# Optimization experiments

Hardware: AMD Instinct MI355X
Metric: run time of the kernel (lower is better)

Reference implementation:

```python
import jax, jax.numpy as jnp
import numpy as np

B, S, H = 2, 1024, 2048
NH, NKV, HD = 16, 4, 128           # heads, kv heads, head_dim
E, TOPK, NG, TOPKG, M = 8, 2, 4, 2, 512  # experts, top_k, n_group, topk_group, moe ffn dim
EPS = 1e-6
THETA = 10000.0
SCALE = HD ** -0.5
RSF = 1.0  # routed_scaling_factor


def rmsnorm(x, w):
    xf = x.astype(jnp.float32)
    var = jnp.mean(xf * xf, axis=-1, keepdims=True)
    return (w * (xf * jax.lax.rsqrt(var + EPS))).astype(x.dtype)


def rotate_half(x):
    x1, x2 = jnp.split(x, 2, axis=-1)
    return jnp.concatenate([-x2, x1], axis=-1)


def setup_inputs() -> dict:
    key = jax.random.key(0)
    ks = jax.random.split(key, 16)
    s = 0.02
    hidden_states = jax.random.normal(ks[0], (B, S, H), jnp.float32)
    pos = jnp.arange(S, dtype=jnp.float32)
    inv_freq = 1.0 / (THETA ** (jnp.arange(0, HD, 2, dtype=jnp.float32) / HD))
    freqs = jnp.outer(pos, inv_freq)                       # [S, HD/2]
    emb = jnp.concatenate([freqs, freqs], axis=-1)         # [S, HD]
    cos = jnp.broadcast_to(jnp.cos(emb)[None], (B, S, HD))
    sin = jnp.broadcast_to(jnp.sin(emb)[None], (B, S, HD))
    return {
        "hidden_states": hidden_states,
        "cos": cos,
        "sin": sin,
        "ln1_w": jnp.ones((H,), jnp.float32),
        "w_qkv": jax.random.normal(ks[1], ((NH + 2 * NKV) * HD, H), jnp.float32) * s,
        "q_ln_w": jnp.ones((HD,), jnp.float32),
        "k_ln_w": jnp.ones((HD,), jnp.float32),
        "w_dense": jax.random.normal(ks[2], (H, NH * HD), jnp.float32) * s,
        "ln2_w": jnp.ones((H,), jnp.float32),
        "gate_w": jax.random.normal(ks[3], (E, H), jnp.float32) * s,
        "gate_bias": jnp.zeros((E,), jnp.float32),
        "we_gate": jax.random.normal(ks[4], (E, M, H), jnp.float32) * s,
        "we_up": jax.random.normal(ks[5], (E, M, H), jnp.float32) * s,
        "we_down": jax.random.normal(ks[6], (E, H, M), jnp.float32) * s,
        "ws_gate": jax.random.normal(ks[7], (M, H), jnp.float32) * s,
        "ws_up": jax.random.normal(ks[8], (M, H), jnp.float32) * s,
        "ws_down": jax.random.normal(ks[9], (H, M), jnp.float32) * s,
    }


def reference(hidden_states, cos, sin, ln1_w, w_qkv, q_ln_w, k_ln_w, w_dense,
              ln2_w, gate_w, gate_bias, we_gate, we_up, we_down,
              ws_gate, ws_up, ws_down):
    # ---- attention block ----
    residual = hidden_states
    x = rmsnorm(hidden_states, ln1_w)
    qkv = jnp.einsum('bsh,oh->bso', x, w_qkv).reshape(B, S, NH + 2 * NKV, HD)
    q, k, v = jnp.split(qkv, [NH, NH + NKV], axis=2)
    q = q.transpose(0, 2, 1, 3)   # [B, NH,  S, HD]
    k = k.transpose(0, 2, 1, 3)   # [B, NKV, S, HD]
    v = v.transpose(0, 2, 1, 3)
    q = rmsnorm(q, q_ln_w)
    k = rmsnorm(k, k_ln_w)
    c, sn = cos[:, None], sin[:, None]  # [B,1,S,HD]
    q = q * c + rotate_half(q) * sn
    k = k * c + rotate_half(k) * sn
    n_rep = NH // NKV
    k = jnp.repeat(k, n_rep, axis=1)
    v = jnp.repeat(v, n_rep, axis=1)
    scores = jnp.einsum('bhqd,bhkd->bhqk', q, k) * SCALE
    attn = jax.nn.softmax(scores.astype(jnp.float32), axis=-1).astype(q.dtype)
    out = jnp.einsum('bhqk,bhkd->bhqd', attn, v)
    out = out.transpose(0, 2, 1, 3).reshape(B, S, NH * HD)
    attn_out = jnp.einsum('bso,ho->bsh', out, w_dense)
    hidden = residual + attn_out

    # ---- MoE block ----
    residual = hidden
    x = rmsnorm(hidden, ln2_w).reshape(B * S, H)
    T = B * S
    logits = jnp.einsum('th,eh->te', x.astype(jnp.float32), gate_w.astype(jnp.float32))
    scores = jax.nn.sigmoid(logits)
    scores_b = scores + gate_bias
    # group-limited routing: pick topk_group groups by sum of top-2 scores per group
    gsz = E // NG
    grp = scores_b.reshape(T, NG, gsz)
    top2 = jax.lax.top_k(grp, min(2, gsz))[0].sum(-1)      # [T, NG]
    _, gidx = jax.lax.top_k(top2, TOPKG)                   # [T, TOPKG]
    gmask = jnp.zeros((T, NG), scores.dtype).at[jnp.arange(T)[:, None], gidx].set(1.0)
    emask = jnp.repeat(gmask, gsz, axis=-1)                # [T, E]
    masked = jnp.where(emask > 0, scores_b, -jnp.inf)
    _, tidx = jax.lax.top_k(masked, TOPK)                  # [T, TOPK]
    tw = jnp.take_along_axis(scores, tidx, axis=-1)
    tw = tw / (tw.sum(-1, keepdims=True) + 1e-20) * RSF
    route = jnp.zeros((T, E), x.dtype).at[jnp.arange(T)[:, None], tidx].set(tw.astype(x.dtype))
    # dense all-expert compute, combined by (sparse) routing weights
    g = jnp.einsum('th,emh->tem', x, we_gate)
    u = jnp.einsum('th,emh->tem', x, we_up)
    he = jax.nn.silu(g) * u
    oe = jnp.einsum('tem,ehm->teh', he, we_down)
    moe = jnp.einsum('te,teh->th', route, oe)
    # shared expert
    sh = jnp.einsum('th,oh->to', jax.nn.silu(x @ ws_gate.T) * (x @ ws_up.T), ws_down)
    out = residual + (moe + sh).reshape(B, S, H)
    return out
```

## Files before the change

kernel.cpp:

```cpp
#include <hip/hip_runtime.h>
#include <cstdint>
#include <cstddef>

#define T_TOK 2048
#define H_DIM 2048
#define S_LEN 1024
#define HD 128
#define NH 16
#define NKV 4
#define QKV_O 3072
#define MM 512
#define EPS 1e-6f
#define ATT_SCALE 0.08838834764831845f

typedef __bf16 bf16x8 __attribute__((ext_vector_type(8)));
typedef __bf16 bf16x4 __attribute__((ext_vector_type(4)));
typedef float  f32x4  __attribute__((ext_vector_type(4)));

__device__ __forceinline__ __bf16 f2bf(float f) {
  unsigned u = __builtin_bit_cast(unsigned, f);
  u += 0x7fffu + ((u >> 16) & 1u);
  unsigned short h = (unsigned short)(u >> 16);
  return __builtin_bit_cast(__bf16, h);
}
__device__ __forceinline__ f32x4 fzero4() {
  f32x4 z; z[0] = 0.f; z[1] = 0.f; z[2] = 0.f; z[3] = 0.f; return z;
}
__device__ __forceinline__ void gld16(const __bf16* g, __bf16* l) {
  __builtin_amdgcn_global_load_lds(
      (const __attribute__((address_space(1))) unsigned int*)g,
      (__attribute__((address_space(3))) unsigned int*)l, 16, 0, 0);
}

__global__ __launch_bounds__(256) void wconv_k(
    const float* __restrict__ s0, const float* __restrict__ s1,
    const float* __restrict__ s2, const float* __restrict__ s3,
    const float* __restrict__ s4, const float* __restrict__ s5,
    const float* __restrict__ s6, const float* __restrict__ s7,
    __bf16* __restrict__ dst) {
  size_t e = ((size_t)blockIdx.x * 256 + threadIdx.x) * 16;
  const size_t E0 = 6291456, E1 = 10485760, E2 = 18874368, E3 = 27262976,
               E4 = 35651584, E5 = 36700160, E6 = 37748736;
  const float* src; size_t base;
  if      (e < E0) { src = s0; base = 0;  }
  else if (e < E1) { src = s1; base = E0; }
  else if (e < E2) { src = s2; base = E1; }
  else if (e < E3) { src = s3; base = E2; }
  else if (e < E4) { src = s4; base = E3; }
  else if (e < E5) { src = s5; base = E4; }
  else if (e < E6) { src = s6; base = E5; }
  else             { src = s7; base = E6; }
  const float4* sp = (const float4*)(src + (e - base));
  float4 f0 = sp[0], f1 = sp[1], f2 = sp[2], f3 = sp[3];
  bf16x8 o0, o1;
  o0[0] = f2bf(f0.x); o0[1] = f2bf(f0.y); o0[2] = f2bf(f0.z); o0[3] = f2bf(f0.w);
  o0[4] = f2bf(f1.x); o0[5] = f2bf(f1.y); o0[6] = f2bf(f1.z); o0[7] = f2bf(f1.w);
  o1[0] = f2bf(f2.x); o1[1] = f2bf(f2.y); o1[2] = f2bf(f2.z); o1[3] = f2bf(f2.w);
  o1[4] = f2bf(f3.x); o1[5] = f2bf(f3.y); o1[6] = f2bf(f3.z); o1[7] = f2bf(f3.w);
  *(bf16x8*)(dst + e) = o0;
  *(bf16x8*)(dst + e + 8) = o1;
}

__global__ __launch_bounds__(256) void rmsnorm_k(const float* __restrict__ X,
                                                 const float* __restrict__ W,
                                                 __bf16* __restrict__ Y) {
  int t = blockIdx.x;
  int tid = threadIdx.x, lane = tid & 63, wid = tid >> 6;
  const float4* row = (const float4*)(X + (size_t)t * H_DIM);
  float4 v0 = row[tid], v1 = row[tid + 256];
  float ss = v0.x*v0.x + v0.y*v0.y + v0.z*v0.z + v0.w*v0.w
           + v1.x*v1.x + v1.y*v1.y + v1.z*v1.z + v1.w*v1.w;
  #pragma unroll
  for (int m = 1; m <= 32; m <<= 1) ss += __shfl_xor(ss, m, 64);
  __shared__ float red[4];
  if (lane == 0) red[wid] = ss;
  __syncthreads();
  float tot = red[0] + red[1] + red[2] + red[3];
  float sc = rsqrtf(tot * (1.f / H_DIM) + EPS);
  const float4* wp = (const float4*)W;
  float4 w0 = wp[tid], w1 = wp[tid + 256];
  bf16x4 o;
  o[0] = f2bf(v0.x*w0.x*sc); o[1] = f2bf(v0.y*w0.y*sc);
  o[2] = f2bf(v0.z*w0.z*sc); o[3] = f2bf(v0.w*w0.w*sc);
  *(bf16x4*)&Y[(size_t)t*H_DIM + tid*4] = o;
  o[0] = f2bf(v1.x*w1.x*sc); o[1] = f2bf(v1.y*w1.y*sc);
  o[2] = f2bf(v1.z*w1.z*sc); o[3] = f2bf(v1.w*w1.w*sc);
  *(bf16x4*)&Y[(size_t)t*H_DIM + 1024 + tid*4] = o;
}

template<int MODE>
__global__ __launch_bounds__(256) void gemm64_nt(
    const __bf16* __restrict__ A, const __bf16* __restrict__ B,
    float* __restrict__ C, __bf16* __restrict__ OB,
    const float* __restrict__ resid, int N, int K) {
  int m0 = blockIdx.y * 64;
  int n0 = blockIdx.x * 128;
  __shared__ __bf16 sA[2][64 * 64];
  __shared__ __bf16 sB[2][128 * 64];
  int tid = threadIdx.x, lane = tid & 63, wid = tid >> 6;
  int quad = lane >> 4, l16 = lane & 15;
  int wm = wid & 1, wn = wid >> 1;

  const __bf16* gA[2]; const __bf16* gB[4];
  #pragma unroll
  for (int i = 0; i < 2; i++) {
    int p = tid + 256 * i;
    int row = p >> 3, sc = p & 7, gc = sc ^ (row & 7);
    gA[i] = A + (size_t)(m0 + row) * K + gc * 8;
  }
  #pragma unroll
  for (int i = 0; i < 4; i++) {
    int p = tid + 256 * i;
    int row = p >> 3, sc = p & 7, gc = sc ^ (row & 7);
    gB[i] = B + (size_t)(n0 + row) * K + gc * 8;
  }
  f32x4 acc[2][4];
  #pragma unroll
  for (int i = 0; i < 2; i++)
    #pragma unroll
    for (int j = 0; j < 4; j++) acc[i][j] = fzero4();

  auto stage = [&](int buf, int k0) {
    #pragma unroll
    for (int i = 0; i < 2; i++)
      gld16(gA[i] + k0, &sA[buf][(tid + 256 * i) * 8]);
    #pragma unroll
    for (int i = 0; i < 4; i++)
      gld16(gB[i] + k0, &sB[buf][(tid + 256 * i) * 8]);
  };
  stage(0, 0);
  int cur = 0;
  for (int k0 = 0; k0 < K; k0 += 64) {
    __syncthreads();
    if (k0 + 64 < K) stage(cur ^ 1, k0 + 64);
    #pragma unroll
    for (int ks = 0; ks < 64; ks += 32) {
      int cb = ks >> 3;
      bf16x8 aF[2], bF[4];
      #pragma unroll
      for (int mt = 0; mt < 2; mt++) {
        int row = wm * 32 + mt * 16 + l16;
        int pos = row * 8 + ((cb + quad) ^ (row & 7));
        aF[mt] = *(const bf16x8*)&sA[cur][pos * 8];
      }
      #pragma unroll
      for (int nt = 0; nt < 4; nt++) {
        int row = wn * 64 + nt * 16 + l16;
        int pos = row * 8 + ((cb + quad) ^ (row & 7));
        bF[nt] = *(const bf16x8*)&sB[cur][pos * 8];
      }
      #pragma unroll
      for (int mt = 0; mt < 2; mt++)
        #pragma unroll
        for (int nt = 0; nt < 4; nt++)
          acc[mt][nt] = __builtin_amdgcn_mfma_f32_16x16x32_bf16(
              aF[mt], bF[nt], acc[mt][nt], 0, 0, 0);
    }
    cur ^= 1;
  }
  #pragma unroll
  for (int mt = 0; mt < 2; mt++) {
    #pragma unroll
    for (int nt = 0; nt < 4; nt++) {
      #pragma unroll
      for (int r = 0; r < 4; r++) {
        int grow = m0 + wm*32 + mt*16 + quad*4 + r;
        int gcol = n0 + wn*64 + nt*16 + l16;
        float val = acc[mt][nt][r];
        if (MODE == 0) {
          OB[(size_t)grow * N + gcol] = f2bf(val);
        } else {
          C[(size_t)grow * H_DIM + gcol] = val + resid[(size_t)grow * H_DIM + gcol];
        }
      }
    }
  }
}

__global__ __launch_bounds__(256) void gemm_down(
    const __bf16* __restrict__ A, const __bf16* __restrict__ B,
    const __bf16* __restrict__ B2, __bf16* __restrict__ OB,
    const int* __restrict__ list, const signed char* __restrict__ jsl,
    const int* __restrict__ cnt) {
  int e  = blockIdx.z;
  int ne = (e == 8) ? T_TOK : cnt[e];
  int m0 = blockIdx.y * 128;
  if (m0 >= ne) return;
  int n0 = blockIdx.x * 128;
  const __bf16* Ab = A + (size_t)e * T_TOK * MM;
  const __bf16* Bb = (e < 8) ? B + (size_t)e * H_DIM * MM : B2;
  const int K = MM;
  __shared__ __bf16 sA[2][128 * 64];
  __shared__ __bf16 sB[2][128 * 64];
  int tid = threadIdx.x, lane = tid & 63, wid = tid >> 6;
  int quad = lane >> 4, l16 = lane & 15;
  int wm = wid & 1, wn = wid >> 1;

  const __bf16* gA[4]; const __bf16* gB[4];
  #pragma unroll
  for (int i = 0; i < 4; i++) {
    int p = tid + 256 * i;
    int row = p >> 3, sc = p & 7, gc = sc ^ (row & 7);
    gA[i] = Ab + (size_t)(m0 + row) * K + gc * 8;
    gB[i] = Bb + (size_t)(n0 + row) * K + gc * 8;
  }
  f32x4 acc[4][4];
  #pragma unroll
  for (int i = 0; i < 4; i++)
    #pragma unroll
    for (int j = 0; j < 4; j++) acc[i][j] = fzero4();

  auto stage = [&](int buf, int k0) {
    #pragma unroll
    for (int i = 0; i < 4; i++) {
      gld16(gA[i] + k0, &sA[buf][(tid + 256 * i) * 8]);
      gld16(gB[i] + k0, &sB[buf][(tid + 256 * i) * 8]);
    }
  };
  stage(0, 0);
  int cur = 0;
  for (int k0 = 0; k0 < K; k0 += 64) {
    __syncthreads();
    if (k0 + 64 < K) stage(cur ^ 1, k0 + 64);
    #pragma unroll
    for (int ks = 0; ks < 64; ks += 32) {
      int cb = ks >> 3;
      bf16x8 aF[4], bF[4];
      #pragma unroll
      for (int mt = 0; mt < 4; mt++) {
        int row = wm * 64 + mt * 16 + l16;
        int pos = row * 8 + ((cb + quad) ^ (row & 7));
        aF[mt] = *(const bf16x8*)&sA[cur][pos * 8];
      }
      #pragma unroll
      for (int nt = 0; nt < 4; nt++) {
        int row = wn * 64 + nt * 16 + l16;
        int pos = row * 8 + ((cb + quad) ^ (row & 7));
        bF[nt] = *(const bf16x8*)&sB[cur][pos * 8];
      }
      #pragma unroll
      for (int mt = 0; mt < 4; mt++)
        #pragma unroll
        for (int nt = 0; nt < 4; nt++)
          acc[mt][nt] = __builtin_amdgcn_mfma_f32_16x16x32_bf16(
              aF[mt], bF[nt], acc[mt][nt], 0, 0, 0);
    }
    cur ^= 1;
  }
  #pragma unroll
  for (int mt = 0; mt < 4; mt++) {
    #pragma unroll
    for (int nt = 0; nt < 4; nt++) {
      #pragma unroll
      for (int r = 0; r < 4; r++) {
        int grow = m0 + wm*64 + mt*16 + quad*4 + r;
        int gcol = n0 + wn*64 + nt*16 + l16;
        if (grow < ne) {
          int tk = list[e * T_TOK + grow];
          int j  = (e == 8) ? 2 : (int)jsl[e * T_TOK + grow];
          OB[((size_t)tk * 3 + j) * H_DIM + gcol] = f2bf(acc[mt][nt][r]);
        }
      }
    }
  }
}

__global__ __launch_bounds__(256) void combine_k(const __bf16* __restrict__ buf,
                                                 float* __restrict__ out) {
  int t = blockIdx.x, tid = threadIdx.x;
  const __bf16* base = buf + (size_t)t * 3 * H_DIM;
  bf16x8 v0 = *(const bf16x8*)(base + tid * 8);
  bf16x8 v1 = *(const bf16x8*)(base + H_DIM + tid * 8);
  bf16x8 v2 = *(const bf16x8*)(base + 2 * H_DIM + tid * 8);
  float* o = out + (size_t)t * H_DIM + tid * 8;
  float4 a = *(float4*)o, b = *(float4*)(o + 4);
  a.x += (float)v0[0] + (float)v1[0] + (float)v2[0];
  a.y += (float)v0[1] + (float)v1[1] + (float)v2[1];
  a.z += (float)v0[2] + (float)v1[2] + (float)v2[2];
  a.w += (float)v0[3] + (float)v1[3] + (float)v2[3];
  b.x += (float)v0[4] + (float)v1[4] + (float)v2[4];
  b.y += (float)v0[5] + (float)v1[5] + (float)v2[5];
  b.z += (float)v0[6] + (float)v1[6] + (float)v2[6];
  b.w += (float)v0[7] + (float)v1[7] + (float)v2[7];
  *(float4*)o = a; *(float4*)(o + 4) = b;
}

__global__ __launch_bounds__(256) void rope_k(
    const __bf16* __restrict__ qkv, const float* __restrict__ qlw,
    const float* __restrict__ klw, const float* __restrict__ cosp,
    const float* __restrict__ sinp, __bf16* __restrict__ qb,
    __bf16* __restrict__ kb, __bf16* __restrict__ vb) {
  int bid = blockIdx.x;
  int t = bid / 6;
  int head = (bid % 6) * 4 + (threadIdx.x >> 6);
  int b = t >> 10, s = t & 1023;
  int d = threadIdx.x & 63;
  const __bf16* src = qkv + (size_t)t * QKV_O + head * HD;
  float x1 = (float)src[d], x2 = (float)src[d + 64];
  if (head < 20) {
    float ssq = x1*x1 + x2*x2;
    #pragma unroll
    for (int m = 1; m <= 32; m <<= 1) ssq += __shfl_xor(ssq, m, 64);
    float sc = rsqrtf(ssq * (1.f / HD) + EPS);
    const float* w = (head < 16) ? qlw : klw;
    x1 = x1 * sc * w[d];
    x2 = x2 * sc * w[d + 64];
    size_t cb = (size_t)t * HD;
    float c1 = cosp[cb + d], s1 = sinp[cb + d];
    float c2 = cosp[cb + d + 64], s2 = sinp[cb + d + 64];
    float o1 = x1 * c1 - x2 * s1;
    float o2 = x2 * c2 + x1 * s2;
    if (head < 16) {
      __bf16* dst = qb + (((size_t)(b * NH + head)) * S_LEN + s) * HD;
      dst[d] = f2bf(o1); dst[d + 64] = f2bf(o2);
    } else {
      int kv = head - 16;
      __bf16* dst = kb + (((size_t)(b * NKV + kv)) * S_LEN + s) * HD;
      dst[d] = f2bf(o1); dst[d + 64] = f2bf(o2);
    }
  } else {
    int kv = head - 20;
    __bf16* dst = vb + (((size_t)(b * NKV + kv)) * S_LEN + s) * HD;
    dst[d] = src[d]; dst[d + 64] = src[d + 64];
  }
}

__global__ __launch_bounds__(256) void vtrans_k(const __bf16* __restrict__ vb,
                                                __bf16* __restrict__ vt) {
  int s0 = blockIdx.x * 64, d0 = blockIdx.y * 64, g = blockIdx.z;
  __shared__ __bf16 sT[64 * 80];
  int tid = threadIdx.x;
  const __bf16* src = vb + (size_t)g * S_LEN * HD;
  #pragma unroll
  for (int i = 0; i < 2; i++) {
    int p = tid + 256 * i;
    int rs = p >> 3, cc = p & 7;
    bf16x8 v = *(const bf16x8*)(src + (size_t)(s0 + rs) * HD + d0 + cc * 8);
    #pragma unroll
    for (int j = 0; j < 8; j++) sT[(cc * 8 + j) * 80 + rs] = v[j];
  }
  __syncthreads();
  __bf16* dst = vt + (size_t)g * HD * S_LEN;
  #pragma unroll
  for (int i = 0; i < 2; i++) {
    int p = tid + 256 * i;
    int rd = p >> 3, cs = p & 7;
    bf16x8 v = *(const bf16x8*)&sT[rd * 80 + cs * 8];
    *(bf16x8*)(dst + (size_t)(d0 + rd) * S_LEN + s0 + cs * 8) = v;
  }
}

__global__ __launch_bounds__(256) void flash_k(
    const __bf16* __restrict__ qb, const __bf16* __restrict__ kb,
    const __bf16* __restrict__ vt, __bf16* __restrict__ outb) {
  int qt = blockIdx.x, bh = blockIdx.y;
  int b = bh >> 4, h = bh & 15, kv = h >> 2;
  int tid = threadIdx.x, lane = tid & 63, wid = tid >> 6;
  int quad = lane >> 4, l16 = lane & 15;
  __shared__ __bf16 sQ[64 * 128];
  __shared__ __bf16 sKP[64 * 128];
  __shared__ __bf16 sVt[128 * 64];
  __bf16* sK = sKP;
  __bf16* sP = sKP;

  const __bf16* qsrc = qb + (((size_t)(b * NH + h)) * S_LEN + qt * 64) * HD;
  #pragma unroll
  for (int i = 0; i < 4; i++) {
    int p = tid + 256 * i;
    int row = p >> 4, sc = p & 15, gc = sc ^ (row & 7);
    gld16(qsrc + (size_t)row * HD + gc * 8, &sQ[p * 8]);
  }
  const __bf16* kbase  = kb + ((size_t)(b * NKV + kv)) * S_LEN * HD;
  const __bf16* vtbase = vt + ((size_t)(b * NKV + kv)) * HD * S_LEN;
  const __bf16* gK[4]; const __bf16* gV[4];
  #pragma unroll
  for (int i = 0; i < 4; i++) {
    int p = tid + 256 * i;
    int rowk = p >> 4, sck = p & 15, gck = sck ^ (rowk & 7);
    gK[i] = kbase + (size_t)rowk * HD + gck * 8;
    int rowv = p >> 3, scv = p & 7, gcv = scv ^ (rowv & 7);
    gV[i] = vtbase + (size_t)rowv * S_LEN + gcv * 8;
  }
  float mrow[4], lrow[4];
  #pragma unroll
  for (int r = 0; r < 4; r++) { mrow[r] = -__builtin_inff(); lrow[r] = 0.f; }
  f32x4 accO[8];
  #pragma unroll
  for (int i = 0; i < 8; i++) accO[i] = fzero4();

  for (int kt = 0; kt < 16; kt++) {
    __syncthreads();
    #pragma unroll
    for (int i = 0; i < 4; i++) {
      gld16(gK[i] + (size_t)kt * 64 * HD, &sK[(tid + 256 * i) * 8]);
      gld16(gV[i] + kt * 64, &sVt[(tid + 256 * i) * 8]);
    }
    __syncthreads();
    f32x4 accS[4];
    #pragma unroll
    for (int jt = 0; jt < 4; jt++) accS[jt] = fzero4();
    int rowA = wid * 16 + l16;
    #pragma unroll
    for (int ks2 = 0; ks2 < 4; ks2++) {
      int posA = rowA * 16 + ((ks2 * 4 + quad) ^ (rowA & 7));
      bf16x8 aF = *(const bf16x8*)&sQ[posA * 8];
      #pragma unroll
      for (int jt = 0; jt < 4; jt++) {
        int rowB = jt * 16 + l16;
        int posB = rowB * 16 + ((ks2 * 4 + quad) ^ (rowB & 7));
        bf16x8 bF = *(const bf16x8*)&sK[posB * 8];
        accS[jt] = __builtin_amdgcn_mfma_f32_16x16x32_bf16(aF, bF, accS[jt], 0, 0, 0);
      }
    }
    float alpha[4];
    #pragma unroll
    for (int r = 0; r < 4; r++) {
      float mx = -__builtin_inff();
      #pragma unroll
      for (int jt = 0; jt < 4; jt++) {
        accS[jt][r] *= ATT_SCALE;
        mx = fmaxf(mx, accS[jt][r]);
      }
      #pragma unroll
      for (int m = 1; m <= 8; m <<= 1) mx = fmaxf(mx, __shfl_xor(mx, m, 64));
      float mn = fmaxf(mrow[r], mx);
      float al = __expf(mrow[r] - mn);
      float rs = 0.f;
      #pragma unroll
      for (int jt = 0; jt < 4; jt++) {
        float p = __expf(accS[jt][r] - mn);
        accS[jt][r] = p;
        rs += p;
      }
      #pragma unroll
      for (int m = 1; m <= 8; m <<= 1) rs += __shfl_xor(rs, m, 64);
      lrow[r] = lrow[r] * al + rs;
      mrow[r] = mn;
      alpha[r] = al;
    }
    #pragma unroll
    for (int nt = 0; nt < 8; nt++)
      #pragma unroll
      for (int r = 0; r < 4; r++) accO[nt][r] *= alpha[r];
    __syncthreads();
    #pragma unroll
    for (int jt = 0; jt < 4; jt++)
      #pragma unroll
      for (int r = 0; r < 4; r++)
        sP[(wid * 16 + quad * 4 + r) * 72 + jt * 16 + l16] = f2bf(accS[jt][r]);
    __syncthreads();
    #pragma unroll
    for (int ks2 = 0; ks2 < 2; ks2++) {
      bf16x8 aF = *(const bf16x8*)&sP[(wid * 16 + l16) * 72 + ks2 * 32 + quad * 8];
      #pragma unroll
      for (int nt = 0; nt < 8; nt++) {
        int rowB = nt * 16 + l16;
        int posB = rowB * 8 + ((ks2 * 4 + quad) ^ (rowB & 7));
        bf16x8 bF = *(const bf16x8*)&sVt[posB * 8];
        accO[nt] = __builtin_amdgcn_mfma_f32_16x16x32_bf16(aF, bF, accO[nt], 0, 0, 0);
      }
    }
  }
  #pragma unroll
  for (int nt = 0; nt < 8; nt++) {
    #pragma unroll
    for (int r = 0; r < 4; r++) {
      int srow = qt * 64 + wid * 16 + quad * 4 + r;
      float val = accO[nt][r] / lrow[r];
      outb[((size_t)(b * S_LEN + srow)) * H_DIM + h * HD + nt * 16 + l16] = f2bf(val);
    }
  }
}

__global__ __launch_bounds__(256) void router_k(
    const float* __restrict__ hid, const float* __restrict__ ln2w,
    const float* __restrict__ gw, const float* __restrict__ gb,
    int* __restrict__ cnt, int* __restrict__ list, float* __restrict__ wsl,
    signed char* __restrict__ jsl) {
  int t = blockIdx.x;
  int tid = threadIdx.x, lane = tid & 63, wid = tid >> 6;
  const float4* row = (const float4*)(hid + (size_t)t * H_DIM);
  float4 v0 = row[tid], v1 = row[tid + 256];
  float ss = v0.x*v0.x + v0.y*v0.y + v0.z*v0.z + v0.w*v0.w
           + v1.x*v1.x + v1.y*v1.y + v1.z*v1.z + v1.w*v1.w;
  #pragma unroll
  for (int m = 1; m <= 32; m <<= 1) ss += __shfl_xor(ss, m, 64);
  __shared__ float red[4];
  __shared__ float lred[4][8];
  if (lane == 0) red[wid] = ss;
  __syncthreads();
  float tot = red[0] + red[1] + red[2] + red[3];
  float sc = rsqrtf(tot * (1.f / H_DIM) + EPS);
  const float4* wp = (const float4*)ln2w;
  float4 w0 = wp[tid], w1 = wp[tid + 256];
  float x0 = v0.x*w0.x*sc, x1 = v0.y*w0.y*sc, x2 = v0.z*w0.z*sc, x3 = v0.w*w0.w*sc;
  float x4 = v1.x*w1.x*sc, x5 = v1.y*w1.y*sc, x6 = v1.z*w1.z*sc, x7 = v1.w*w1.w*sc;
  float pe[8];
  #pragma unroll
  for (int e = 0; e < 8; e++) {
    const float4* gp = (const float4*)(gw + (size_t)e * H_DIM);
    float4 g0 = gp[tid], g1 = gp[tid + 256];
    float d = x0*g0.x + x1*g0.y + x2*g0.z + x3*g0.w
            + x4*g1.x + x5*g1.y + x6*g1.z + x7*g1.w;
    #pragma unroll
    for (int m = 1; m <= 32; m <<= 1) d += __shfl_xor(d, m, 64);
    pe[e] = d;
  }
  if (lane == 0) {
    #pragma unroll
    for (int e = 0; e < 8; e++) lred[wid][e] = pe[e];
  }
  __syncthreads();
  if (tid == 0) {
    float s[8], sb[8];
    #pragma unroll
    for (int e = 0; e < 8; e++) {
      float lg = lred[0][e] + lred[1][e] + lred[2][e] + lred[3][e];
      s[e] = 1.f / (1.f + __expf(-lg));
      sb[e] = s[e] + gb[e];
    }
    float gs[4];
    #pragma unroll
    for (int g = 0; g < 4; g++) gs[g] = sb[2 * g] + sb[2 * g + 1];
    int g1 = 0;
    for (int g = 1; g < 4; g++) if (gs[g] > gs[g1]) g1 = g;
    int g2 = -1;
    for (int g = 0; g < 4; g++) if (g != g1 && (g2 < 0 || gs[g] > gs[g2])) g2 = g;
    unsigned emask = (3u << (2 * g1)) | (3u << (2 * g2));
    int e1 = -1;
    for (int e = 0; e < 8; e++) if (((emask >> e) & 1u) && (e1 < 0 || sb[e] > sb[e1])) e1 = e;
    int e2 = -1;
    for (int e = 0; e < 8; e++) if (((emask >> e) & 1u) && e != e1 && (e2 < 0 || sb[e] > sb[e2])) e2 = e;
    float w1s = s[e1], w2s = s[e2];
    float dn = w1s + w2s + 1e-20f;
    w1s /= dn; w2s /= dn;
    int p1 = atomicAdd(&cnt[e1], 1);
    list[e1 * T_TOK + p1] = t; wsl[e1 * T_TOK + p1] = w1s; jsl[e1 * T_TOK + p1] = 0;
    int p2 = atomicAdd(&cnt[e2], 1);
    list[e2 * T_TOK + p2] = t; wsl[e2 * T_TOK + p2] = w2s; jsl[e2 * T_TOK + p2] = 1;
    list[8 * T_TOK + t] = t; wsl[8 * T_TOK + t] = 1.f;
  }
}

__global__ __launch_bounds__(256) void gemm_gateup(
    const __bf16* __restrict__ X, const __bf16* __restrict__ weg,
    const __bf16* __restrict__ weu, const __bf16* __restrict__ wsg,
    const __bf16* __restrict__ wsu, const int* __restrict__ list,
    const float* __restrict__ wsl, const int* __restrict__ cnt,
    __bf16* __restrict__ he) {
  int e = blockIdx.z;
  int ne = (e == 8) ? T_TOK : cnt[e];
  int m0 = blockIdx.y * 128;
  if (m0 >= ne) return;
  int n0 = blockIdx.x * 64;
  const __bf16* bg = (e < 8) ? weg + (size_t)e * MM * H_DIM : wsg;
  const __bf16* bu = (e < 8) ? weu + (size_t)e * MM * H_DIM : wsu;
  const int* lst = list + e * T_TOK;
  __shared__ __bf16 sA[2][128 * 64];
  __shared__ __bf16 sBg[2][64 * 64];
  __shared__ __bf16 sBu[2][64 * 64];
  int tid = threadIdx.x, lane = tid & 63, wid = tid >> 6;
  int quad = lane >> 4, l16 = lane & 15;

  const __bf16* gA[4]; const __bf16* gBg[2]; const __bf16* gBu[2];
  #pragma unroll
  for (int i = 0; i < 4; i++) {
    int p = tid + 256 * i;
    int row = p >> 3, sc = p & 7, gc = sc ^ (row & 7);
    int r = m0 + row; if (r >= ne) r = ne - 1;
    int tk = lst[r];
    gA[i] = X + (size_t)tk * H_DIM + gc * 8;
  }
  #pragma unroll
  for (int i = 0; i < 2; i++) {
    int p = tid + 256 * i;
    int row = p >> 3, sc = p & 7, gc = sc ^ (row & 7);
    gBg[i] = bg + (size_t)(n0 + row) * H_DIM + gc * 8;
    gBu[i] = bu + (size_t)(n0 + row) * H_DIM + gc * 8;
  }
  f32x4 ag[2][4], au[2][4];
  #pragma unroll
  for (int i = 0; i < 2; i++)
    #pragma unroll
    for (int j = 0; j < 4; j++) { ag[i][j] = fzero4(); au[i][j] = fzero4(); }

  auto stage = [&](int buf, int k0) {
    #pragma unroll
    for (int i = 0; i < 4; i++)
      gld16(gA[i] + k0, &sA[buf][(tid + 256 * i) * 8]);
    #pragma unroll
    for (int i = 0; i < 2; i++) {
      gld16(gBg[i] + k0, &sBg[buf][(tid + 256 * i) * 8]);
      gld16(gBu[i] + k0, &sBu[buf][(tid + 256 * i) * 8]);
    }
  };
  stage(0, 0);
  int cur = 0;
  for (int k0 = 0; k0 < H_DIM; k0 += 64) {
    __syncthreads();
    if (k0 + 64 < H_DIM) stage(cur ^ 1, k0 + 64);
    #pragma unroll
    for (int ks = 0; ks < 64; ks += 32) {
      int cb = ks >> 3;
      bf16x8 aF[2], gF[4], uF[4];
      #pragma unroll
      for (int mt = 0; mt < 2; mt++) {
        int row = wid * 32 + mt * 16 + l16;
        int pos = row * 8 + ((cb + quad) ^ (row & 7));
        aF[mt] = *(const bf16x8*)&sA[cur][pos * 8];
      }
      #pragma unroll
      for (int nt = 0; nt < 4; nt++) {
        int row = nt * 16 + l16;
        int pos = row * 8 + ((cb + quad) ^ (row & 7));
        gF[nt] = *(const bf16x8*)&sBg[cur][pos * 8];
        uF[nt] = *(const bf16x8*)&sBu[cur][pos * 8];
      }
      #pragma unroll
      for (int mt = 0; mt < 2; mt++)
        #pragma unroll
        for (int nt = 0; nt < 4; nt++) {
          ag[mt][nt] = __builtin_amdgcn_mfma_f32_16x16x32_bf16(aF[mt], gF[nt], ag[mt][nt], 0, 0, 0);
          au[mt][nt] = __builtin_amdgcn_mfma_f32_16x16x32_bf16(aF[mt], uF[nt], au[mt][nt], 0, 0, 0);
        }
    }
    cur ^= 1;
  }
  #pragma unroll
  for (int mt = 0; mt < 2; mt++) {
    #pragma unroll
    for (int nt = 0; nt < 4; nt++) {
      #pragma unroll
      for (int r = 0; r < 4; r++) {
        int row_l = wid * 32 + mt * 16 + quad * 4 + r;
        int grow = m0 + row_l;
        if (grow < ne) {
          float g = ag[mt][nt][r], u = au[mt][nt][r];
          float hv = g / (1.f + __expf(-g)) * u;
          hv *= wsl[e * T_TOK + grow];
          he[((size_t)e * T_TOK + grow) * MM + n0 + nt * 16 + l16] = f2bf(hv);
        }
      }
    }
  }
}

extern "C" void kernel_launch(void* const* d_in, const int* in_sizes, int n_in,
                              void* d_out, int out_size, void* d_ws, size_t ws_size,
                              hipStream_t stream) {
  (void)in_sizes; (void)n_in; (void)out_size; (void)ws_size;
  const float* hs     = (const float*)d_in[0];
  const float* cosp   = (const float*)d_in[1];
  const float* sinp   = (const float*)d_in[2];
  const float* ln1w   = (const float*)d_in[3];
  const float* wqkv   = (const float*)d_in[4];
  const float* qlw    = (const float*)d_in[5];
  const float* klw    = (const float*)d_in[6];
  const float* wdense = (const float*)d_in[7];
  const float* ln2w   = (const float*)d_in[8];
  const float* gw     = (const float*)d_in[9];
  const float* gbias  = (const float*)d_in[10];
  const float* weg    = (const float*)d_in[11];
  const float* weu    = (const float*)d_in[12];
  const float* wed    = (const float*)d_in[13];
  const float* wsg    = (const float*)d_in[14];
  const float* wsu    = (const float*)d_in[15];
  const float* wsd    = (const float*)d_in[16];
  float* out = (float*)d_out;

  char* ws = (char*)d_ws;
  size_t off = 0;
  auto alloc = [&](size_t b) { char* p = ws + off; off += (b + 255) & ~(size_t)255; return p; };
  __bf16* wbf   = (__bf16*)alloc((size_t)38797312 * 2);
  __bf16* xb1   = (__bf16*)alloc((size_t)T_TOK * H_DIM * 2);
  __bf16* qreg  = (__bf16*)alloc((size_t)T_TOK * 3 * H_DIM * 2);
  __bf16* qb    = (__bf16*)alloc((size_t)2 * NH  * S_LEN * HD * 2);
  __bf16* kb    = (__bf16*)alloc((size_t)2 * NKV * S_LEN * HD * 2);
  __bf16* vb    = (__bf16*)alloc((size_t)2 * NKV * S_LEN * HD * 2);
  __bf16* vt    = (__bf16*)alloc((size_t)2 * NKV * S_LEN * HD * 2);
  __bf16* outb  = (__bf16*)alloc((size_t)T_TOK * H_DIM * 2);
  __bf16* xb2   = (__bf16*)alloc((size_t)T_TOK * H_DIM * 2);
  int*    cnt   = (int*)   alloc(256);
  int*    list  = (int*)   alloc((size_t)9 * T_TOK * 4);
  float*  wsl   = (float*) alloc((size_t)9 * T_TOK * 4);
  signed char* jsl = (signed char*)alloc((size_t)9 * T_TOK);
  __bf16* qkvb  = qreg;
  __bf16* buf   = qreg;
  __bf16* he    = qb;

  const __bf16* wqkv_bf   = wbf;
  const __bf16* wdense_bf = wbf + 6291456;
  const __bf16* weg_bf    = wbf + 10485760;
  const __bf16* weu_bf    = wbf + 18874368;
  const __bf16* wed_bf    = wbf + 27262976;
  const __bf16* wsg_bf    = wbf + 35651584;
  const __bf16* wsu_bf    = wbf + 36700160;
  const __bf16* wsd_bf    = wbf + 37748736;

  hipMemsetAsync(cnt, 0, 256, stream);
  wconv_k<<<9472, 256, 0, stream>>>(wqkv, wdense, weg, weu, wed, wsg, wsu, wsd, wbf);
  rmsnorm_k<<<T_TOK, 256, 0, stream>>>(hs, ln1w, xb1);
  gemm64_nt<0><<<dim3(QKV_O / 128, T_TOK / 64), 256, 0, stream>>>(
      xb1, wqkv_bf, nullptr, qkvb, nullptr, QKV_O, H_DIM);
  rope_k<<<T_TOK * 6, 256, 0, stream>>>(qkvb, qlw, klw, cosp, sinp, qb, kb, vb);
  vtrans_k<<<dim3(16, 2, 8), 256, 0, stream>>>(vb, vt);
  flash_k<<<dim3(S_LEN / 64, 2 * NH), 256, 0, stream>>>(qb, kb, vt, outb);
  gemm64_nt<1><<<dim3(H_DIM / 128, T_TOK / 64), 256, 0, stream>>>(
      outb, wdense_bf, out, nullptr, hs, H_DIM, H_DIM);
  rmsnorm_k<<<T_TOK, 256, 0, stream>>>(out, ln2w, xb2);
  router_k<<<T_TOK, 256, 0, stream>>>(out, ln2w, gw, gbias, cnt, list, wsl, jsl);
  gemm_gateup<<<dim3(MM / 64, T_TOK / 128, 9), 256, 0, stream>>>(
      xb2, weg_bf, weu_bf, wsg_bf, wsu_bf, list, wsl, cnt, he);
  gemm_down<<<dim3(H_DIM / 128, T_TOK / 128, 9), 256, 0, stream>>>(
      he, wed_bf, wsd_bf, buf, list, jsl, cnt);
  combine_k<<<T_TOK, 256, 0, stream>>>(buf, out);
}
```

Before: 500.6 us.

## Convert MoE expert weights to bf16 inside GEMMs instead of a separate pass

The standalone weight-conversion kernel now converts only the QKV and dense weights. The MoE gate/up/down and shared-expert GEMMs read fp32 weights directly into registers, convert them to bf16 and write them to shared memory after the MFMA loop of each k-step. This removes a full fp32 read plus bf16 write and re-read of roughly 28M weight elements. In exchange the GEMMs read twice the bytes per weight tile, re-read each weight tile across M-tiles, and lose the async global-to-LDS path for B.

```diff
diff --git a/kernel.cpp b/kernel.cpp
--- a/kernel.cpp
+++ b/kernel.cpp
@@ -34,22 +34,12 @@
 
 __global__ __launch_bounds__(256) void wconv_k(
     const float* __restrict__ s0, const float* __restrict__ s1,
-    const float* __restrict__ s2, const float* __restrict__ s3,
-    const float* __restrict__ s4, const float* __restrict__ s5,
-    const float* __restrict__ s6, const float* __restrict__ s7,
     __bf16* __restrict__ dst) {
   size_t e = ((size_t)blockIdx.x * 256 + threadIdx.x) * 16;
-  const size_t E0 = 6291456, E1 = 10485760, E2 = 18874368, E3 = 27262976,
-               E4 = 35651584, E5 = 36700160, E6 = 37748736;
+  const size_t E0 = 6291456;
   const float* src; size_t base;
-  if      (e < E0) { src = s0; base = 0;  }
-  else if (e < E1) { src = s1; base = E0; }
-  else if (e < E2) { src = s2; base = E1; }
-  else if (e < E3) { src = s3; base = E2; }
-  else if (e < E4) { src = s4; base = E3; }
-  else if (e < E5) { src = s5; base = E4; }
-  else if (e < E6) { src = s6; base = E5; }
-  else             { src = s7; base = E6; }
+  if (e < E0) { src = s0; base = 0; }
+  else        { src = s1; base = E0; }
   const float4* sp = (const float4*)(src + (e - base));
   float4 f0 = sp[0], f1 = sp[1], f2 = sp[2], f3 = sp[3];
   bf16x8 o0, o1;
@@ -178,8 +168,8 @@
 }
 
 __global__ __launch_bounds__(256) void gemm_down(
-    const __bf16* __restrict__ A, const __bf16* __restrict__ B,
-    const __bf16* __restrict__ B2, __bf16* __restrict__ OB,
+    const __bf16* __restrict__ A, const float* __restrict__ B,
+    const float* __restrict__ B2, __bf16* __restrict__ OB,
     const int* __restrict__ list, const signed char* __restrict__ jsl,
     const int* __restrict__ cnt) {
   int e  = blockIdx.z;
@@ -188,7 +178,7 @@
   if (m0 >= ne) return;
   int n0 = blockIdx.x * 128;
   const __bf16* Ab = A + (size_t)e * T_TOK * MM;
-  const __bf16* Bb = (e < 8) ? B + (size_t)e * H_DIM * MM : B2;
+  const float*  Bb = (e < 8) ? B + (size_t)e * H_DIM * MM : B2;
   const int K = MM;
   __shared__ __bf16 sA[2][128 * 64];
   __shared__ __bf16 sB[2][128 * 64];
@@ -196,7 +186,7 @@
   int quad = lane >> 4, l16 = lane & 15;
   int wm = wid & 1, wn = wid >> 1;
 
-  const __bf16* gA[4]; const __bf16* gB[4];
+  const __bf16* gA[4]; const float* gB[4];
   #pragma unroll
   for (int i = 0; i < 4; i++) {
     int p = tid + 256 * i;
@@ -210,18 +200,35 @@
     #pragma unroll
     for (int j = 0; j < 4; j++) acc[i][j] = fzero4();
 
-  auto stage = [&](int buf, int k0) {
+  f32x4 br[4][2];
+  auto stageA = [&](int buf, int k0) {
+    #pragma unroll
+    for (int i = 0; i < 4; i++)
+      gld16(gA[i] + k0, &sA[buf][(tid + 256 * i) * 8]);
+  };
+  auto loadB = [&](int k0) {
     #pragma unroll
     for (int i = 0; i < 4; i++) {
-      gld16(gA[i] + k0, &sA[buf][(tid + 256 * i) * 8]);
-      gld16(gB[i] + k0, &sB[buf][(tid + 256 * i) * 8]);
+      br[i][0] = *(const f32x4*)(gB[i] + k0);
+      br[i][1] = *(const f32x4*)(gB[i] + k0 + 4);
     }
   };
-  stage(0, 0);
+  auto writeB = [&](int buf) {
+    #pragma unroll
+    for (int i = 0; i < 4; i++) {
+      int p = tid + 256 * i;
+      bf16x8 o;
+      #pragma unroll
+      for (int j = 0; j < 4; j++) { o[j] = f2bf(br[i][0][j]); o[j+4] = f2bf(br[i][1][j]); }
+      *(bf16x8*)&sB[buf][p * 8] = o;
+    }
+  };
+  stageA(0, 0); loadB(0); writeB(0);
   int cur = 0;
   for (int k0 = 0; k0 < K; k0 += 64) {
     __syncthreads();
-    if (k0 + 64 < K) stage(cur ^ 1, k0 + 64);
+    bool nxt = (k0 + 64 < K);
+    if (nxt) { stageA(cur ^ 1, k0 + 64); loadB(k0 + 64); }
     #pragma unroll
     for (int ks = 0; ks < 64; ks += 32) {
       int cb = ks >> 3;
@@ -245,6 +252,7 @@
           acc[mt][nt] = __builtin_amdgcn_mfma_f32_16x16x32_bf16(
               aF[mt], bF[nt], acc[mt][nt], 0, 0, 0);
     }
+    if (nxt) writeB(cur ^ 1);
     cur ^= 1;
   }
   #pragma unroll
@@ -543,9 +551,9 @@
 }
 
 __global__ __launch_bounds__(256) void gemm_gateup(
-    const __bf16* __restrict__ X, const __bf16* __restrict__ weg,
-    const __bf16* __restrict__ weu, const __bf16* __restrict__ wsg,
-    const __bf16* __restrict__ wsu, const int* __restrict__ list,
+    const __bf16* __restrict__ X, const float* __restrict__ weg,
+    const float* __restrict__ weu, const float* __restrict__ wsg,
+    const float* __restrict__ wsu, const int* __restrict__ list,
     const float* __restrict__ wsl, const int* __restrict__ cnt,
     __bf16* __restrict__ he) {
   int e = blockIdx.z;
@@ -553,8 +561,8 @@
   int m0 = blockIdx.y * 128;
   if (m0 >= ne) return;
   int n0 = blockIdx.x * 64;
-  const __bf16* bg = (e < 8) ? weg + (size_t)e * MM * H_DIM : wsg;
-  const __bf16* bu = (e < 8) ? weu + (size_t)e * MM * H_DIM : wsu;
+  const float* bg = (e < 8) ? weg + (size_t)e * MM * H_DIM : wsg;
+  const float* bu = (e < 8) ? weu + (size_t)e * MM * H_DIM : wsu;
   const int* lst = list + e * T_TOK;
   __shared__ __bf16 sA[2][128 * 64];
   __shared__ __bf16 sBg[2][64 * 64];
@@ -562,7 +570,7 @@
   int tid = threadIdx.x, lane = tid & 63, wid = tid >> 6;
   int quad = lane >> 4, l16 = lane & 15;
 
-  const __bf16* gA[4]; const __bf16* gBg[2]; const __bf16* gBu[2];
+  const __bf16* gA[4]; const float* gBg[2]; const float* gBu[2];
   #pragma unroll
   for (int i = 0; i < 4; i++) {
     int p = tid + 256 * i;
@@ -584,21 +592,41 @@
     #pragma unroll
     for (int j = 0; j < 4; j++) { ag[i][j] = fzero4(); au[i][j] = fzero4(); }
 
-  auto stage = [&](int buf, int k0) {
+  f32x4 bgr[2][2], bur[2][2];
+  auto stageA = [&](int buf, int k0) {
     #pragma unroll
     for (int i = 0; i < 4; i++)
       gld16(gA[i] + k0, &sA[buf][(tid + 256 * i) * 8]);
+  };
+  auto loadB = [&](int k0) {
     #pragma unroll
     for (int i = 0; i < 2; i++) {
-      gld16(gBg[i] + k0, &sBg[buf][(tid + 256 * i) * 8]);
-      gld16(gBu[i] + k0, &sBu[buf][(tid + 256 * i) * 8]);
+      bgr[i][0] = *(const f32x4*)(gBg[i] + k0);
+      bgr[i][1] = *(const f32x4*)(gBg[i] + k0 + 4);
+      bur[i][0] = *(const f32x4*)(gBu[i] + k0);
+      bur[i][1] = *(const f32x4*)(gBu[i] + k0 + 4);
     }
   };
-  stage(0, 0);
+  auto writeB = [&](int buf) {
+    #pragma unroll
+    for (int i = 0; i < 2; i++) {
+      int p = tid + 256 * i;
+      bf16x8 og, ou;
+      #pragma unroll
+      for (int j = 0; j < 4; j++) {
+        og[j] = f2bf(bgr[i][0][j]); og[j+4] = f2bf(bgr[i][1][j]);
+        ou[j] = f2bf(bur[i][0][j]); ou[j+4] = f2bf(bur[i][1][j]);
+      }
+      *(bf16x8*)&sBg[buf][p * 8] = og;
+      *(bf16x8*)&sBu[buf][p * 8] = ou;
+    }
+  };
+  stageA(0, 0); loadB(0); writeB(0);
   int cur = 0;
   for (int k0 = 0; k0 < H_DIM; k0 += 64) {
     __syncthreads();
-    if (k0 + 64 < H_DIM) stage(cur ^ 1, k0 + 64);
+    bool nxt = (k0 + 64 < H_DIM);
+    if (nxt) { stageA(cur ^ 1, k0 + 64); loadB(k0 + 64); }
     #pragma unroll
     for (int ks = 0; ks < 64; ks += 32) {
       int cb = ks >> 3;
@@ -624,6 +652,7 @@
           au[mt][nt] = __builtin_amdgcn_mfma_f32_16x16x32_bf16(aF[mt], uF[nt], au[mt][nt], 0, 0, 0);
         }
     }
+    if (nxt) writeB(cur ^ 1);
     cur ^= 1;
   }
   #pragma unroll
@@ -671,7 +700,7 @@
   char* ws = (char*)d_ws;
   size_t off = 0;
   auto alloc = [&](size_t b) { char* p = ws + off; off += (b + 255) & ~(size_t)255; return p; };
-  __bf16* wbf   = (__bf16*)alloc((size_t)38797312 * 2);
+  __bf16* wbf   = (__bf16*)alloc((size_t)10485760 * 2);
   __bf16* xb1   = (__bf16*)alloc((size_t)T_TOK * H_DIM * 2);
   __bf16* qreg  = (__bf16*)alloc((size_t)T_TOK * 3 * H_DIM * 2);
   __bf16* qb    = (__bf16*)alloc((size_t)2 * NH  * S_LEN * HD * 2);
@@ -690,15 +719,9 @@
 
   const __bf16* wqkv_bf   = wbf;
   const __bf16* wdense_bf = wbf + 6291456;
-  const __bf16* weg_bf    = wbf + 10485760;
-  const __bf16* weu_bf    = wbf + 18874368;
-  const __bf16* wed_bf    = wbf + 27262976;
-  const __bf16* wsg_bf    = wbf + 35651584;
-  const __bf16* wsu_bf    = wbf + 36700160;
-  const __bf16* wsd_bf    = wbf + 37748736;
 
   hipMemsetAsync(cnt, 0, 256, stream);
-  wconv_k<<<9472, 256, 0, stream>>>(wqkv, wdense, weg, weu, wed, wsg, wsu, wsd, wbf);
+  wconv_k<<<2560, 256, 0, stream>>>(wqkv, wdense, wbf);
   rmsnorm_k<<<T_TOK, 256, 0, stream>>>(hs, ln1w, xb1);
   gemm64_nt<0><<<dim3(QKV_O / 128, T_TOK / 64), 256, 0, stream>>>(
       xb1, wqkv_bf, nullptr, qkvb, nullptr, QKV_O, H_DIM);
@@ -710,8 +733,8 @@
   rmsnorm_k<<<T_TOK, 256, 0, stream>>>(out, ln2w, xb2);
   router_k<<<T_TOK, 256, 0, stream>>>(out, ln2w, gw, gbias, cnt, list, wsl, jsl);
   gemm_gateup<<<dim3(MM / 64, T_TOK / 128, 9), 256, 0, stream>>>(
-      xb2, weg_bf, weu_bf, wsg_bf, wsu_bf, list, wsl, cnt, he);
+      xb2, weg, weu, wsg, wsu, list, wsl, cnt, he);
   gemm_down<<<dim3(H_DIM / 128, T_TOK / 128, 9), 256, 0, stream>>>(
-      he, wed_bf, wsd_bf, buf, list, jsl, cnt);
+      he, wed, wsd, buf, list, jsl, cnt);
   combine_k<<<T_TOK, 256, 0, stream>>>(buf, out);
 }
```

Measured after the change: 508.6 us. About the same (+1.6%).
